# Kernel optimization log

Hardware: AMD Instinct MI355X
Metric: run time of the kernel (lower is better)

## Reference

```python
import jax, jax.numpy as jnp
import numpy as np

N, E = 30000, 480000
IN_DIM, HID, HEADS, OUT_DIM, EDIM = 128, 64, 4, 32, 1
NEG_SLOPE = 0.2
EPS_BN = 1e-5


def segment_softmax(logits, seg, num_segments):
    m = jax.ops.segment_max(logits, seg, num_segments=num_segments)
    ex = jnp.exp(logits - m[seg])
    s = jax.ops.segment_sum(ex, seg, num_segments=num_segments)
    return ex / (s[seg] + 1e-16)


def gat_layer(x, src, dst, ea, W, We, a_s, a_d, a_e, b):
    # PyG GATConv: shared lin for src/dst, edge_dim attention, softmax over dst
    n = x.shape[0]
    H, D = a_s.shape
    h = (x @ W).reshape(n, H, D)                      # [N,H,D]
    e = (ea @ We).reshape(-1, H, D)                   # [E,H,D]
    logits = (h * a_s).sum(-1)[src] + (h * a_d).sum(-1)[dst] + (e * a_e).sum(-1)
    alpha = segment_softmax(jax.nn.leaky_relu(logits, NEG_SLOPE), dst, n)  # [E,H]
    out = jax.ops.segment_sum(alpha[:, :, None] * h[src], dst, num_segments=n)
    return out.reshape(n, H * D) + b


def setup_inputs() -> dict:
    key = jax.random.key(0)
    ks = jax.random.split(key, 24)
    s = 0.1
    return {
        "x": jax.random.normal(ks[0], (N, IN_DIM), jnp.float32),
        "edge_attr": jax.random.uniform(ks[1], (E, EDIM), jnp.float32),
        "bn_gamma": jnp.ones((EDIM,), jnp.float32),
        "bn_beta": jnp.zeros((EDIM,), jnp.float32),
        "W1": s * jax.random.normal(ks[2], (IN_DIM, HEADS * HID), jnp.float32),
        "We1": s * jax.random.normal(ks[3], (EDIM, HEADS * HID), jnp.float32),
        "a_src1": s * jax.random.normal(ks[4], (HEADS, HID), jnp.float32),
        "a_dst1": s * jax.random.normal(ks[5], (HEADS, HID), jnp.float32),
        "a_edge1": s * jax.random.normal(ks[6], (HEADS, HID), jnp.float32),
        "b1": jnp.zeros((HEADS * HID,), jnp.float32),
        "W2": s * jax.random.normal(ks[7], (HEADS * HID, OUT_DIM), jnp.float32),
        "We2": s * jax.random.normal(ks[8], (EDIM, OUT_DIM), jnp.float32),
        "a_src2": s * jax.random.normal(ks[9], (1, OUT_DIM), jnp.float32),
        "a_dst2": s * jax.random.normal(ks[10], (1, OUT_DIM), jnp.float32),
        "a_edge2": s * jax.random.normal(ks[11], (1, OUT_DIM), jnp.float32),
        "b2": jnp.zeros((OUT_DIM,), jnp.float32),
        "dec_W1": s * jax.random.normal(ks[12], (OUT_DIM, HID), jnp.float32),
        "dec_b1": jnp.zeros((HID,), jnp.float32),
        "dec_W2": s * jax.random.normal(ks[13], (HID, IN_DIM), jnp.float32),
        "dec_b2": jnp.zeros((IN_DIM,), jnp.float32),
        "edge_index": jax.random.randint(ks[14], (2, E), 0, N, dtype=jnp.int32),
    }


def reference(x, edge_attr, bn_gamma, bn_beta, W1, We1, a_src1, a_dst1, a_edge1, b1,
              W2, We2, a_src2, a_dst2, a_edge2, b2, dec_W1, dec_b1, dec_W2, dec_b2,
              edge_index):
    n = x.shape[0]
    src, dst = edge_index[0], edge_index[1]
    # BatchNorm1d (batch stats, biased var) on log1p(edge_attr)
    ea = jnp.log1p(edge_attr)
    mu = ea.mean(0)
    var = ea.var(0)
    ea = (ea - mu) / jnp.sqrt(var + EPS_BN) * bn_gamma + bn_beta
    # add_self_loops with fill_value='mean' (mean of incoming edge attrs per node)
    ones = jnp.ones((src.shape[0],), ea.dtype)
    cnt = jax.ops.segment_sum(ones, dst, num_segments=n)
    loop_attr = jax.ops.segment_sum(ea, dst, num_segments=n) / jnp.maximum(cnt, 1.0)[:, None]
    ar = jnp.arange(n)
    src2 = jnp.concatenate([src, ar])
    dst2 = jnp.concatenate([dst, ar])
    ea2 = jnp.concatenate([ea, loop_attr], axis=0)
    # encoder: 2-layer GAT (eval mode: dropout is identity)
    h = jax.nn.elu(gat_layer(x, src2, dst2, ea2, W1, We1, a_src1, a_dst1, a_edge1, b1))
    z = gat_layer(h, src2, dst2, ea2, W2, We2, a_src2, a_dst2, a_edge2, b2)
    # feature decoder MLP
    x_hat = jax.nn.elu(z @ dec_W1 + dec_b1) @ dec_W2 + dec_b2
    return z, x_hat
```

## Files before the change

### kernel.cpp

```cpp
#include <hip/hip_runtime.h>
#include <math.h>

#define NN 30000
#define EE 480000
#define NEG_SLOPE 0.2f
#define LDK 136
#define LDK2 264
#define CAP 64
#define NPB 1875

static const size_t I_FILL  = 0;
static const size_t F_PART  = 30000;
static const size_t F_SCAL  = 34096;
static const size_t F_WTB   = 34112;
static const size_t F_WT2B  = 50496;
static const size_t F_HB    = 54592;
static const size_t F_S1    = 3894592;
static const size_t F_D1    = 4014592;
static const size_t F_H1B   = 4134592;
static const size_t F_H2    = 7974592;
static const size_t F_S2    = 8934592;
static const size_t F_D2    = 8964592;
static const size_t I_ER    = 8994592;

typedef __attribute__((ext_vector_type(4))) float f32x4;
typedef __attribute__((ext_vector_type(8))) short bf16x8;

__device__ __forceinline__ float wsum64(float v) {
    #pragma unroll
    for (int o = 32; o; o >>= 1) v += __shfl_xor(v, o);
    return v;
}
__device__ __forceinline__ unsigned int pack_bf2(float a, float b) {
    unsigned int ua = __float_as_uint(a);
    unsigned int ub = __float_as_uint(b);
    ua = (ua + 0x7FFFu + ((ua >> 16) & 1u)) >> 16;
    ub = (ub + 0x7FFFu + ((ub >> 16) & 1u)) & 0xFFFF0000u;
    return ua | ub;
}
__device__ __forceinline__ unsigned short bf16r(float f) {
    unsigned int u = __float_as_uint(f);
    u = (u + 0x7FFFu + ((u >> 16) & 1u)) >> 16;
    return (unsigned short)u;
}
__device__ __forceinline__ float bflo(unsigned int u) { return __uint_as_float(u << 16); }
__device__ __forceinline__ float bfhi(unsigned int u) { return __uint_as_float(u & 0xFFFF0000u); }

__global__ __launch_bounds__(256) void k_prepw(const float* __restrict__ W1,
        const float* __restrict__ W2, unsigned short* __restrict__ wtb,
        unsigned short* __restrict__ wt2b, int* __restrict__ fill) {
    int idx = blockIdx.x * 256 + threadIdx.x;
    if (idx < NN) fill[idx] = 0;
    if (idx < 128 * 256) {
        int k = idx >> 8, n = idx & 255;
        wtb[n * 128 + k] = bf16r(W1[idx]);
    } else if (idx < 128 * 256 + 256 * 32) {
        int i2 = idx - 128 * 256;
        int k = i2 >> 5, c = i2 & 31;
        wt2b[c * 256 + k] = bf16r(W2[i2]);
    }
}

__global__ __launch_bounds__(256) void k_scatter(const int* __restrict__ src,
        const int* __restrict__ dst, const float* __restrict__ eattr,
        int* __restrict__ fill, uint2* __restrict__ er,
        float* __restrict__ part, int E) {
    __shared__ float sa[256], sb[256];
    int tid = threadIdx.x;
    int e = blockIdx.x * 256 + tid;
    float s = 0.f, s2 = 0.f;
    if (e < E) {
        float lv = log1pf(eattr[e]);
        s = lv; s2 = lv * lv;
        int d = dst[e];
        int pos = atomicAdd(&fill[d], 1);
        if (pos > CAP - 2) pos = CAP - 2;
        er[d * CAP + pos] = make_uint2((unsigned int)src[e], __float_as_uint(lv));
    }
    sa[tid] = s; sb[tid] = s2;
    __syncthreads();
    for (int o = 128; o; o >>= 1) {
        if (tid < o) { sa[tid] += sa[tid + o]; sb[tid] += sb[tid + o]; }
        __syncthreads();
    }
    if (tid == 0) { part[blockIdx.x * 2] = sa[0]; part[blockIdx.x * 2 + 1] = sb[0]; }
}

__global__ __launch_bounds__(512) void k_bn_final(const float* __restrict__ part,
        const float* __restrict__ gamma, const float* __restrict__ beta,
        const float* __restrict__ We1, const float* __restrict__ ae1,
        const float* __restrict__ We2, const float* __restrict__ ae2,
        float* __restrict__ scal, int E) {
    __shared__ float sa[512], sb[512], sc[256];
    int tid = threadIdx.x;
    float s = 0.f, s2 = 0.f;
    for (int i = tid; i < NPB; i += 512) {
        s += part[2 * i]; s2 += part[2 * i + 1];
    }
    sa[tid] = s; sb[tid] = s2;
    if (tid < 256) sc[tid] = We1[tid] * ae1[tid];
    __syncthreads();
    for (int o = 256; o; o >>= 1) {
        if (tid < o) { sa[tid] += sa[tid + o]; sb[tid] += sb[tid + o]; }
        __syncthreads();
    }
    if (tid == 0) {
        float mu = sa[0] / (float)E;
        float var = sb[0] / (float)E - mu * mu;
        float kA = gamma[0] / sqrtf(var + 1e-5f);
        float kB = beta[0] - mu * kA;
        for (int h = 0; h < 4; h++) {
            float s1 = 0.f;
            for (int d = 0; d < 64; d++) s1 += sc[h * 64 + d];
            scal[4 + h] = kA * s1;
            scal[10 + h] = kB * s1;
        }
        float s22 = 0.f;
        for (int d = 0; d < 32; d++) s22 += We2[d] * ae2[d];
        scal[8] = kA * s22;
        scal[9] = kB * s22;
    }
}

__global__ __launch_bounds__(256) void k_gemm1(const float* __restrict__ x,
        const unsigned short* __restrict__ wtb, const float* __restrict__ as1,
        const float* __restrict__ ad1, unsigned short* __restrict__ hb,
        float* __restrict__ s1, float* __restrict__ d1, int M) {
    __shared__ unsigned short xs[32 * LDK];
    __shared__ unsigned short wt[256 * LDK];
    int tid = threadIdx.x;
    int bm = blockIdx.x * 32;
    #pragma unroll
    for (int i = 0; i < 16; i++) {
        int c = tid + i * 256;
        int row = c >> 4, koff = (c & 15) * 8;
        uint4 v = *(const uint4*)&wtb[row * 128 + koff];
        *(uint4*)&wt[row * LDK + koff] = v;
    }
    #pragma unroll
    for (int i = 0; i < 4; i++) {
        int idx = tid + i * 256;
        int row = idx >> 5, c4 = (idx & 31) * 4;
        int grow = bm + row;
        float4 v = make_float4(0.f, 0.f, 0.f, 0.f);
        if (grow < M) v = *(const float4*)&x[grow * 128 + c4];
        uint2 p = make_uint2(pack_bf2(v.x, v.y), pack_bf2(v.z, v.w));
        *(uint2*)&xs[row * LDK + c4] = p;
    }
    __syncthreads();

    int w = tid >> 6;
    int l = tid & 63;
    int l15 = l & 15, lg = l >> 4;

    f32x4 acc[2][4];
    #pragma unroll
    for (int m = 0; m < 2; m++)
        #pragma unroll
        for (int n = 0; n < 4; n++) acc[m][n] = (f32x4){0.f, 0.f, 0.f, 0.f};

    #pragma unroll
    for (int ks = 0; ks < 4; ks++) {
        int k0 = ks * 32 + lg * 8;
        bf16x8 a0 = *(const bf16x8*)&xs[(l15) * LDK + k0];
        bf16x8 a1 = *(const bf16x8*)&xs[(16 + l15) * LDK + k0];
        bf16x8 b[4];
        #pragma unroll
        for (int n = 0; n < 4; n++)
            b[n] = *(const bf16x8*)&wt[(w * 64 + n * 16 + l15) * LDK + k0];
        #pragma unroll
        for (int n = 0; n < 4; n++) {
            acc[0][n] = __builtin_amdgcn_mfma_f32_16x16x32_bf16(a0, b[n], acc[0][n], 0, 0, 0);
            acc[1][n] = __builtin_amdgcn_mfma_f32_16x16x32_bf16(a1, b[n], acc[1][n], 0, 0, 0);
        }
    }

    #pragma unroll
    for (int m = 0; m < 2; m++) {
        #pragma unroll
        for (int r = 0; r < 4; r++) {
            int grow = bm + m * 16 + lg * 4 + r;
            if (grow < M) {
                #pragma unroll
                for (int n = 0; n < 4; n++)
                    hb[grow * 256 + w * 64 + n * 16 + l15] = bf16r(acc[m][n][r]);
            }
        }
    }
    float as_c[4], ad_c[4];
    #pragma unroll
    for (int n = 0; n < 4; n++) {
        as_c[n] = as1[w * 64 + n * 16 + l15];
        ad_c[n] = ad1[w * 64 + n * 16 + l15];
    }
    float sp[2][4], dp[2][4];
    #pragma unroll
    for (int m = 0; m < 2; m++)
        #pragma unroll
        for (int r = 0; r < 4; r++) {
            float s = 0.f, d = 0.f;
            #pragma unroll
            for (int n = 0; n < 4; n++) {
                s += acc[m][n][r] * as_c[n];
                d += acc[m][n][r] * ad_c[n];
            }
            sp[m][r] = s; dp[m][r] = d;
        }
    #pragma unroll
    for (int o = 1; o < 16; o <<= 1) {
        #pragma unroll
        for (int m = 0; m < 2; m++)
            #pragma unroll
            for (int r = 0; r < 4; r++) {
                sp[m][r] += __shfl_xor(sp[m][r], o);
                dp[m][r] += __shfl_xor(dp[m][r], o);
            }
    }
    if (l15 == 0) {
        #pragma unroll
        for (int m = 0; m < 2; m++)
            #pragma unroll
            for (int r = 0; r < 4; r++) {
                int grow = bm + m * 16 + lg * 4 + r;
                if (grow < M) {
                    s1[grow * 4 + w] = sp[m][r];
                    d1[grow * 4 + w] = dp[m][r];
                }
            }
    }
}

__global__ __launch_bounds__(256) void k_agg1(const int* __restrict__ fill,
        const uint2* __restrict__ er, const float* __restrict__ s1,
        const float* __restrict__ d1, const float* __restrict__ scal,
        const unsigned short* __restrict__ hb, const float* __restrict__ b1,
        unsigned short* __restrict__ h1b, int N) {
    __shared__ float sma[4][256];
    __shared__ int   sms[4][64];
    int wid = threadIdx.x >> 6;
    int node = blockIdx.x * 4 + wid;
    if (node >= N) return;
    int lane = threadIdx.x & 63;
    int deg = fill[node]; if (deg > 63) deg = 63;
    float4 dv = *(const float4*)&d1[node * 4];
    float4 ce = *(const float4*)&scal[4];
    float4 cc = *(const float4*)&scal[10];

    uint2 e = make_uint2((unsigned int)node, 0u);
    if (lane < deg) e = er[node * CAP + lane];
    float ev = (lane < deg) ? __uint_as_float(e.y) : 0.f;
    float evm = wsum64(ev) / fmaxf((float)deg, 1.f);
    int degT = deg + 1;
    if (lane == deg) ev = evm;
    bool valid = lane < degT;

    float4 l = make_float4(-1e30f, -1e30f, -1e30f, -1e30f);
    if (valid) {
        float4 sv = *(const float4*)&s1[e.x * 4];
        l.x = sv.x + dv.x + ev * ce.x + cc.x;
        l.y = sv.y + dv.y + ev * ce.y + cc.y;
        l.z = sv.z + dv.z + ev * ce.z + cc.z;
        l.w = sv.w + dv.w + ev * ce.w + cc.w;
        l.x = l.x > 0.f ? l.x : NEG_SLOPE * l.x;
        l.y = l.y > 0.f ? l.y : NEG_SLOPE * l.y;
        l.z = l.z > 0.f ? l.z : NEG_SLOPE * l.z;
        l.w = l.w > 0.f ? l.w : NEG_SLOPE * l.w;
    }
    float4 mx = l;
    #pragma unroll
    for (int o = 32; o; o >>= 1) {
        mx.x = fmaxf(mx.x, __shfl_xor(mx.x, o));
        mx.y = fmaxf(mx.y, __shfl_xor(mx.y, o));
        mx.z = fmaxf(mx.z, __shfl_xor(mx.z, o));
        mx.w = fmaxf(mx.w, __shfl_xor(mx.w, o));
    }
    float4 ex = make_float4(0.f, 0.f, 0.f, 0.f);
    if (valid) {
        ex.x = __expf(l.x - mx.x); ex.y = __expf(l.y - mx.y);
        ex.z = __expf(l.z - mx.z); ex.w = __expf(l.w - mx.w);
    }
    float4 sm = ex;
    #pragma unroll
    for (int o = 32; o; o >>= 1) {
        sm.x += __shfl_xor(sm.x, o); sm.y += __shfl_xor(sm.y, o);
        sm.z += __shfl_xor(sm.z, o); sm.w += __shfl_xor(sm.w, o);
    }
    *(float4*)&sma[wid][lane * 4] = make_float4(ex.x, ex.y, ex.z, ex.w);
    sms[wid][lane] = (int)e.x;
    int p = lane >> 5;
    int dL = lane & 31;
    int h = dL >> 3;
    float acc[8];
    #pragma unroll
    for (int i = 0; i < 8; i++) acc[i] = 0.f;
    for (int c0 = 0; c0 < degT; c0 += 8) {
        int sv[4]; float av[4];
        #pragma unroll
        for (int t = 0; t < 4; t++) {
            int ee = c0 + 2 * t + p;
            sv[t] = sms[wid][ee];
            av[t] = sma[wid][ee * 4 + h];
        }
        uint4 hv[4];
        #pragma unroll
        for (int t = 0; t < 4; t++)
            hv[t] = *(const uint4*)&hb[(unsigned)sv[t] * 256 + dL * 8];
        #pragma unroll
        for (int t = 0; t < 4; t++) {
            float a = av[t];
            acc[0] += a * bflo(hv[t].x); acc[1] += a * bfhi(hv[t].x);
            acc[2] += a * bflo(hv[t].y); acc[3] += a * bfhi(hv[t].y);
            acc[4] += a * bflo(hv[t].z); acc[5] += a * bfhi(hv[t].z);
            acc[6] += a * bflo(hv[t].w); acc[7] += a * bfhi(hv[t].w);
        }
    }
    #pragma unroll
    for (int i = 0; i < 8; i++) acc[i] += __shfl_xor(acc[i], 32);
    float smh = h == 0 ? sm.x : h == 1 ? sm.y : h == 2 ? sm.z : sm.w;
    float invh = 1.f / (smh + 1e-16f);
    float4 bb0 = *(const float4*)&b1[dL * 8];
    float4 bb1 = *(const float4*)&b1[dL * 8 + 4];
    float r[8];
    r[0] = acc[0] * invh + bb0.x; r[1] = acc[1] * invh + bb0.y;
    r[2] = acc[2] * invh + bb0.z; r[3] = acc[3] * invh + bb0.w;
    r[4] = acc[4] * invh + bb1.x; r[5] = acc[5] * invh + bb1.y;
    r[6] = acc[6] * invh + bb1.z; r[7] = acc[7] * invh + bb1.w;
    #pragma unroll
    for (int i = 0; i < 8; i++)
        r[i] = r[i] > 0.f ? r[i] : (__expf(r[i]) - 1.f);
    if (p == 0) {
        uint4 pk;
        pk.x = pack_bf2(r[0], r[1]); pk.y = pack_bf2(r[2], r[3]);
        pk.z = pack_bf2(r[4], r[5]); pk.w = pack_bf2(r[6], r[7]);
        *(uint4*)&h1b[node * 256 + dL * 8] = pk;
    }
}

__global__ __launch_bounds__(256) void k_gemm2(const unsigned short* __restrict__ h1b,
        const unsigned short* __restrict__ wt2b, const float* __restrict__ as2,
        const float* __restrict__ ad2, float* __restrict__ h2,
        float* __restrict__ s2, float* __restrict__ d2, int M) {
    __shared__ unsigned short h1s[64 * LDK2];
    __shared__ unsigned short w2s[32 * LDK2];
    int tid = threadIdx.x;
    int bm = blockIdx.x * 64;
    #pragma unroll
    for (int i = 0; i < 8; i++) {
        int c = tid + i * 256;
        int row = c >> 5, off = (c & 31) * 8;
        int grow = bm + row;
        uint4 v = make_uint4(0u, 0u, 0u, 0u);
        if (grow < M) v = *(const uint4*)&h1b[grow * 256 + off];
        *(uint4*)&h1s[row * LDK2 + off] = v;
    }
    #pragma unroll
    for (int i = 0; i < 4; i++) {
        int c = tid + i * 256;
        int row = c >> 5, off = (c & 31) * 8;
        uint4 v = *(const uint4*)&wt2b[row * 256 + off];
        *(uint4*)&w2s[row * LDK2 + off] = v;
    }
    __syncthreads();

    int w = tid >> 6;
    int l = tid & 63;
    int l15 = l & 15, lg = l >> 4;

    f32x4 acc0 = (f32x4){0.f, 0.f, 0.f, 0.f};
    f32x4 acc1 = (f32x4){0.f, 0.f, 0.f, 0.f};
    #pragma unroll
    for (int ks = 0; ks < 8; ks++) {
        int k0 = ks * 32 + lg * 8;
        bf16x8 a = *(const bf16x8*)&h1s[(w * 16 + l15) * LDK2 + k0];
        bf16x8 b0 = *(const bf16x8*)&w2s[(l15) * LDK2 + k0];
        bf16x8 b1 = *(const bf16x8*)&w2s[(16 + l15) * LDK2 + k0];
        acc0 = __builtin_amdgcn_mfma_f32_16x16x32_bf16(a, b0, acc0, 0, 0, 0);
        acc1 = __builtin_amdgcn_mfma_f32_16x16x32_bf16(a, b1, acc1, 0, 0, 0);
    }

    #pragma unroll
    for (int r = 0; r < 4; r++) {
        int grow = bm + w * 16 + lg * 4 + r;
        if (grow < M) {
            h2[grow * 32 + l15] = acc0[r];
            h2[grow * 32 + 16 + l15] = acc1[r];
        }
    }
    float sc0 = as2[l15], sc1 = as2[16 + l15];
    float dc0 = ad2[l15], dc1 = ad2[16 + l15];
    #pragma unroll
    for (int r = 0; r < 4; r++) {
        float sp = acc0[r] * sc0 + acc1[r] * sc1;
        float dp = acc0[r] * dc0 + acc1[r] * dc1;
        #pragma unroll
        for (int o = 1; o < 16; o <<= 1) {
            sp += __shfl_xor(sp, o);
            dp += __shfl_xor(dp, o);
        }
        if (l15 == 0) {
            int grow = bm + w * 16 + lg * 4 + r;
            if (grow < M) { s2[grow] = sp; d2[grow] = dp; }
        }
    }
}

__global__ __launch_bounds__(256) void k_agg2(const int* __restrict__ fill,
        const uint2* __restrict__ er, const float* __restrict__ s2,
        const float* __restrict__ d2, const float* __restrict__ scal,
        const float* __restrict__ h2, const float* __restrict__ b2,
        float* __restrict__ zout, int N) {
    __shared__ float sa2[4][64];
    __shared__ int   ss2[4][64];
    int wid = threadIdx.x >> 6;
    int node = blockIdx.x * 4 + wid;
    if (node >= N) return;
    int lane = threadIdx.x & 63;
    int deg = fill[node]; if (deg > 63) deg = 63;
    float dn = d2[node];
    float ce = scal[8], cc = scal[9];

    uint2 e = make_uint2((unsigned int)node, 0u);
    if (lane < deg) e = er[node * CAP + lane];
    float ev = (lane < deg) ? __uint_as_float(e.y) : 0.f;
    float evm = wsum64(ev) / fmaxf((float)deg, 1.f);
    int degT = deg + 1;
    if (lane == deg) ev = evm;
    bool valid = lane < degT;

    float l = -1e30f;
    if (valid) {
        l = s2[e.x] + dn + ev * ce + cc;
        l = l > 0.f ? l : NEG_SLOPE * l;
    }
    float mx = l;
    #pragma unroll
    for (int o = 32; o; o >>= 1) mx = fmaxf(mx, __shfl_xor(mx, o));
    float ex = valid ? __expf(l - mx) : 0.f;
    float sm = wsum64(ex);
    float inv = 1.f / (sm + 1e-16f);
    sa2[wid][lane] = ex;
    ss2[wid][lane] = (int)e.x;
    int p8 = lane >> 3, dL2 = lane & 7;
    float4 acc = make_float4(0.f, 0.f, 0.f, 0.f);
    for (int c0 = 0; c0 < degT; c0 += 32) {
        int sv[4]; float av[4];
        #pragma unroll
        for (int t = 0; t < 4; t++) {
            int ee = c0 + 8 * t + p8;
            sv[t] = ss2[wid][ee];
            av[t] = sa2[wid][ee];
        }
        float4 hv[4];
        #pragma unroll
        for (int t = 0; t < 4; t++)
            hv[t] = *(const float4*)&h2[(unsigned)sv[t] * 32 + dL2 * 4];
        #pragma unroll
        for (int t = 0; t < 4; t++) {
            acc.x += av[t] * hv[t].x; acc.y += av[t] * hv[t].y;
            acc.z += av[t] * hv[t].z; acc.w += av[t] * hv[t].w;
        }
    }
    #pragma unroll
    for (int o = 8; o <= 32; o <<= 1) {
        acc.x += __shfl_xor(acc.x, o); acc.y += __shfl_xor(acc.y, o);
        acc.z += __shfl_xor(acc.z, o); acc.w += __shfl_xor(acc.w, o);
    }
    if (lane < 8) {
        float4 bb = *(const float4*)&b2[dL2 * 4];
        float4 oo;
        oo.x = acc.x * inv + bb.x; oo.y = acc.y * inv + bb.y;
        oo.z = acc.z * inv + bb.z; oo.w = acc.w * inv + bb.w;
        *(float4*)&zout[node * 32 + dL2 * 4] = oo;
    }
}

__global__ __launch_bounds__(256) void k_decoder(const float* __restrict__ z,
        const float* __restrict__ W1, const float* __restrict__ b1,
        const float* __restrict__ W2, const float* __restrict__ b2,
        float* __restrict__ xhat, int M) {
    __shared__ float zs[16][32];
    __shared__ float w1s[32 * 64];
    __shared__ float hid[16][68];
    __shared__ float w2s[64 * 128];
    int tid = threadIdx.x;
    int bn = blockIdx.x * 16;
    #pragma unroll
    for (int i = 0; i < 2; i++) {
        int idx = tid + i * 256;
        int r = idx >> 5, c = idx & 31;
        int row = bn + r;
        zs[r][c] = (row < M) ? z[row * 32 + c] : 0.f;
    }
    #pragma unroll
    for (int i = 0; i < 2; i++) {
        int idx = tid + i * 256;
        int r = idx >> 4, c = (idx & 15) * 4;
        *(float4*)&w1s[r * 64 + c] = *(const float4*)&W1[r * 64 + c];
    }
    #pragma unroll
    for (int i = 0; i < 8; i++) {
        int idx = tid + i * 256;
        int r = idx >> 5, c = (idx & 31) * 4;
        *(float4*)&w2s[r * 128 + c] = *(const float4*)&W2[r * 128 + c];
    }
    __syncthreads();
    {
        int nl = tid >> 4, c0 = (tid & 15) * 4;
        float4 acc = make_float4(0.f, 0.f, 0.f, 0.f);
        #pragma unroll 8
        for (int k = 0; k < 32; k++) {
            float zv = zs[nl][k];
            float4 w = *(float4*)&w1s[k * 64 + c0];
            acc.x += zv * w.x; acc.y += zv * w.y;
            acc.z += zv * w.z; acc.w += zv * w.w;
        }
        float4 bb = *(const float4*)&b1[c0];
        float r0 = acc.x + bb.x, r1 = acc.y + bb.y, r2 = acc.z + bb.z, r3 = acc.w + bb.w;
        r0 = r0 > 0.f ? r0 : (__expf(r0) - 1.f);
        r1 = r1 > 0.f ? r1 : (__expf(r1) - 1.f);
        r2 = r2 > 0.f ? r2 : (__expf(r2) - 1.f);
        r3 = r3 > 0.f ? r3 : (__expf(r3) - 1.f);
        hid[nl][c0] = r0; hid[nl][c0 + 1] = r1; hid[nl][c0 + 2] = r2; hid[nl][c0 + 3] = r3;
    }
    __syncthreads();
    {
        int nl = tid >> 4, c0 = (tid & 15) * 4;
        float acc[8];
        #pragma unroll
        for (int q = 0; q < 8; q++) acc[q] = 0.f;
        #pragma unroll 8
        for (int k = 0; k < 64; k++) {
            float hv = hid[nl][k];
            float4 w0 = *(float4*)&w2s[k * 128 + c0];
            float4 w1 = *(float4*)&w2s[k * 128 + c0 + 64];
            acc[0] += hv * w0.x; acc[1] += hv * w0.y; acc[2] += hv * w0.z; acc[3] += hv * w0.w;
            acc[4] += hv * w1.x; acc[5] += hv * w1.y; acc[6] += hv * w1.z; acc[7] += hv * w1.w;
        }
        int row = bn + nl;
        if (row < M) {
            float4 bb0 = *(const float4*)&b2[c0];
            float4 bb1 = *(const float4*)&b2[c0 + 64];
            float4 o0 = make_float4(acc[0] + bb0.x, acc[1] + bb0.y, acc[2] + bb0.z, acc[3] + bb0.w);
            float4 o1 = make_float4(acc[4] + bb1.x, acc[5] + bb1.y, acc[6] + bb1.z, acc[7] + bb1.w);
            *(float4*)&xhat[row * 128 + c0] = o0;
            *(float4*)&xhat[row * 128 + c0 + 64] = o1;
        }
    }
}

extern "C" void kernel_launch(void* const* d_in, const int* in_sizes, int n_in,
                              void* d_out, int out_size, void* d_ws, size_t ws_size,
                              hipStream_t stream) {
    const float* x        = (const float*)d_in[0];
    const float* eattr    = (const float*)d_in[1];
    const float* bn_gamma = (const float*)d_in[2];
    const float* bn_beta  = (const float*)d_in[3];
    const float* W1       = (const float*)d_in[4];
    const float* We1      = (const float*)d_in[5];
    const float* as1      = (const float*)d_in[6];
    const float* ad1      = (const float*)d_in[7];
    const float* ae1      = (const float*)d_in[8];
    const float* b1       = (const float*)d_in[9];
    const float* W2       = (const float*)d_in[10];
    const float* We2      = (const float*)d_in[11];
    const float* as2      = (const float*)d_in[12];
    const float* ad2      = (const float*)d_in[13];
    const float* ae2      = (const float*)d_in[14];
    const float* b2       = (const float*)d_in[15];
    const float* dW1      = (const float*)d_in[16];
    const float* db1      = (const float*)d_in[17];
    const float* dW2      = (const float*)d_in[18];
    const float* db2      = (const float*)d_in[19];
    const int*   eidx     = (const int*)d_in[20];
    const int* src = eidx;
    const int* dst = eidx + EE;

    float* ws = (float*)d_ws;
    int*   fill = (int*)(ws + I_FILL);
    float* part = ws + F_PART;
    float* scal = ws + F_SCAL;
    unsigned short* wtb  = (unsigned short*)(ws + F_WTB);
    unsigned short* wt2b = (unsigned short*)(ws + F_WT2B);
    unsigned short* hb   = (unsigned short*)(ws + F_HB);
    float* s1   = ws + F_S1;
    float* d1   = ws + F_D1;
    unsigned short* h1b = (unsigned short*)(ws + F_H1B);
    float* h2   = ws + F_H2;
    float* s2   = ws + F_S2;
    float* d2   = ws + F_D2;
    uint2* er   = (uint2*)(ws + I_ER);

    float* zout = (float*)d_out;
    float* xhat = (float*)d_out + NN * 32;

    k_prepw<<<160, 256, 0, stream>>>(W1, W2, wtb, wt2b, fill);
    k_scatter<<<NPB, 256, 0, stream>>>(src, dst, eattr, fill, er, part, EE);
    k_bn_final<<<1, 512, 0, stream>>>(part, bn_gamma, bn_beta, We1, ae1, We2, ae2, scal, EE);
    k_gemm1<<<(NN + 31) / 32, 256, 0, stream>>>(x, wtb, as1, ad1, hb, s1, d1, NN);
    k_agg1<<<(NN + 3) / 4, 256, 0, stream>>>(fill, er, s1, d1, scal, hb, b1, h1b, NN);
    k_gemm2<<<(NN + 63) / 64, 256, 0, stream>>>(h1b, wt2b, as2, ad2, h2, s2, d2, NN);
    k_agg2<<<(NN + 3) / 4, 256, 0, stream>>>(fill, er, s2, d2, scal, h2, b2, zout, NN);
    k_decoder<<<(NN + 15) / 16, 256, 0, stream>>>(zout, dW1, db1, dW2, db2, xhat, NN);
}
```

Measured before the change: 136.5 us.

## Merge edge scatter and first-layer GEMM into one launch via block ranges

Combines the edge scatter/BN-partial kernel and the layer-1 GEMM into a single grid, where the first NPB blocks do the scatter and the remaining blocks do the GEMM. The two independent stages can then overlap on the GPU and one launch disappears. The GEMM also stops staging the whole 256x128 weight tile in LDS and reads B fragments directly from global/L2, which cuts LDS use to raise occupancy. The cost is uncoalesced, repeated global reads of the weights in the MFMA loop.

New measurement: 135.0 us. No clear change (-1.1%).

```diff
diff --git a/kernel.cpp b/kernel.cpp
--- a/kernel.cpp
+++ b/kernel.cpp
@@ -8,6 +8,7 @@
 #define LDK2 264
 #define CAP 64
 #define NPB 1875
+#define NGB 938
 
 static const size_t I_FILL  = 0;
 static const size_t F_PART  = 30000;
@@ -61,29 +62,132 @@
     }
 }
 
-__global__ __launch_bounds__(256) void k_scatter(const int* __restrict__ src,
+__global__ __launch_bounds__(256) void k_scat_gemm(const int* __restrict__ src,
         const int* __restrict__ dst, const float* __restrict__ eattr,
-        int* __restrict__ fill, uint2* __restrict__ er,
-        float* __restrict__ part, int E) {
-    __shared__ float sa[256], sb[256];
+        int* __restrict__ fill, uint2* __restrict__ er, float* __restrict__ part,
+        const float* __restrict__ x, const unsigned short* __restrict__ wtb,
+        const float* __restrict__ as1, const float* __restrict__ ad1,
+        unsigned short* __restrict__ hb, float* __restrict__ s1,
+        float* __restrict__ d1, int E, int M) {
+    __shared__ char shbuf[32 * LDK * 2];
     int tid = threadIdx.x;
-    int e = blockIdx.x * 256 + tid;
-    float s = 0.f, s2 = 0.f;
-    if (e < E) {
-        float lv = log1pf(eattr[e]);
-        s = lv; s2 = lv * lv;
-        int d = dst[e];
-        int pos = atomicAdd(&fill[d], 1);
-        if (pos > CAP - 2) pos = CAP - 2;
-        er[d * CAP + pos] = make_uint2((unsigned int)src[e], __float_as_uint(lv));
-    }
-    sa[tid] = s; sb[tid] = s2;
+
+    if (blockIdx.x < NPB) {
+        float* sa = (float*)shbuf;
+        float* sb = sa + 256;
+        int e = blockIdx.x * 256 + tid;
+        float s = 0.f, s2 = 0.f;
+        if (e < E) {
+            float lv = log1pf(eattr[e]);
+            s = lv; s2 = lv * lv;
+            int d = dst[e];
+            int pos = atomicAdd(&fill[d], 1);
+            if (pos > CAP - 2) pos = CAP - 2;
+            er[d * CAP + pos] = make_uint2((unsigned int)src[e], __float_as_uint(lv));
+        }
+        sa[tid] = s; sb[tid] = s2;
+        __syncthreads();
+        for (int o = 128; o; o >>= 1) {
+            if (tid < o) { sa[tid] += sa[tid + o]; sb[tid] += sb[tid + o]; }
+            __syncthreads();
+        }
+        if (tid == 0) { part[blockIdx.x * 2] = sa[0]; part[blockIdx.x * 2 + 1] = sb[0]; }
+        return;
+    }
+
+    unsigned short* xs = (unsigned short*)shbuf;
+    int bm = (blockIdx.x - NPB) * 32;
+    #pragma unroll
+    for (int i = 0; i < 4; i++) {
+        int idx = tid + i * 256;
+        int row = idx >> 5, c4 = (idx & 31) * 4;
+        int grow = bm + row;
+        float4 v = make_float4(0.f, 0.f, 0.f, 0.f);
+        if (grow < M) v = *(const float4*)&x[grow * 128 + c4];
+        uint2 p = make_uint2(pack_bf2(v.x, v.y), pack_bf2(v.z, v.w));
+        *(uint2*)&xs[row * LDK + c4] = p;
+    }
     __syncthreads();
-    for (int o = 128; o; o >>= 1) {
-        if (tid < o) { sa[tid] += sa[tid + o]; sb[tid] += sb[tid + o]; }
-        __syncthreads();
-    }
-    if (tid == 0) { part[blockIdx.x * 2] = sa[0]; part[blockIdx.x * 2 + 1] = sb[0]; }
+
+    int w = tid >> 6;
+    int l = tid & 63;
+    int l15 = l & 15, lg = l >> 4;
+
+    f32x4 acc[2][4];
+    #pragma unroll
+    for (int m = 0; m < 2; m++)
+        #pragma unroll
+        for (int n = 0; n < 4; n++) acc[m][n] = (f32x4){0.f, 0.f, 0.f, 0.f};
+
+    #pragma unroll
+    for (int ks = 0; ks < 4; ks++) {
+        int k0 = ks * 32 + lg * 8;
+        bf16x8 a0 = *(const bf16x8*)&xs[(l15) * LDK + k0];
+        bf16x8 a1 = *(const bf16x8*)&xs[(16 + l15) * LDK + k0];
+        bf16x8 b[4];
+        #pragma unroll
+        for (int n = 0; n < 4; n++)
+            b[n] = *(const bf16x8*)&wtb[(w * 64 + n * 16 + l15) * 128 + k0];
+        #pragma unroll
+        for (int n = 0; n < 4; n++) {
+            acc[0][n] = __builtin_amdgcn_mfma_f32_16x16x32_bf16(a0, b[n], acc[0][n], 0, 0, 0);
+            acc[1][n] = __builtin_amdgcn_mfma_f32_16x16x32_bf16(a1, b[n], acc[1][n], 0, 0, 0);
+        }
+    }
+
+    #pragma unroll
+    for (int m = 0; m < 2; m++) {
+        #pragma unroll
+        for (int r = 0; r < 4; r++) {
+            int grow = bm + m * 16 + lg * 4 + r;
+            if (grow < M) {
+                #pragma unroll
+                for (int n = 0; n < 4; n++)
+                    hb[grow * 256 + w * 64 + n * 16 + l15] = bf16r(acc[m][n][r]);
+            }
+        }
+    }
+    float as_c[4], ad_c[4];
+    #pragma unroll
+    for (int n = 0; n < 4; n++) {
+        as_c[n] = as1[w * 64 + n * 16 + l15];
+        ad_c[n] = ad1[w * 64 + n * 16 + l15];
+    }
+    float sp[2][4], dp[2][4];
+    #pragma unroll
+    for (int m = 0; m < 2; m++)
+        #pragma unroll
+        for (int r = 0; r < 4; r++) {
+            float s = 0.f, d = 0.f;
+            #pragma unroll
+            for (int n = 0; n < 4; n++) {
+                s += acc[m][n][r] * as_c[n];
+                d += acc[m][n][r] * ad_c[n];
+            }
+            sp[m][r] = s; dp[m][r] = d;
+        }
+    #pragma unroll
+    for (int o = 1; o < 16; o <<= 1) {
+        #pragma unroll
+        for (int m = 0; m < 2; m++)
+            #pragma unroll
+            for (int r = 0; r < 4; r++) {
+                sp[m][r] += __shfl_xor(sp[m][r], o);
+                dp[m][r] += __shfl_xor(dp[m][r], o);
+            }
+    }
+    if (l15 == 0) {
+        #pragma unroll
+        for (int m = 0; m < 2; m++)
+            #pragma unroll
+            for (int r = 0; r < 4; r++) {
+                int grow = bm + m * 16 + lg * 4 + r;
+                if (grow < M) {
+                    s1[grow * 4 + w] = sp[m][r];
+                    d1[grow * 4 + w] = dp[m][r];
+                }
+            }
+    }
 }
 
 __global__ __launch_bounds__(512) void k_bn_final(const float* __restrict__ part,
@@ -119,114 +223,6 @@
         for (int d = 0; d < 32; d++) s22 += We2[d] * ae2[d];
         scal[8] = kA * s22;
         scal[9] = kB * s22;
-    }
-}
-
-__global__ __launch_bounds__(256) void k_gemm1(const float* __restrict__ x,
-        const unsigned short* __restrict__ wtb, const float* __restrict__ as1,
-        const float* __restrict__ ad1, unsigned short* __restrict__ hb,
-        float* __restrict__ s1, float* __restrict__ d1, int M) {
-    __shared__ unsigned short xs[32 * LDK];
-    __shared__ unsigned short wt[256 * LDK];
-    int tid = threadIdx.x;
-    int bm = blockIdx.x * 32;
-    #pragma unroll
-    for (int i = 0; i < 16; i++) {
-        int c = tid + i * 256;
-        int row = c >> 4, koff = (c & 15) * 8;
-        uint4 v = *(const uint4*)&wtb[row * 128 + koff];
-        *(uint4*)&wt[row * LDK + koff] = v;
-    }
-    #pragma unroll
-    for (int i = 0; i < 4; i++) {
-        int idx = tid + i * 256;
-        int row = idx >> 5, c4 = (idx & 31) * 4;
-        int grow = bm + row;
-        float4 v = make_float4(0.f, 0.f, 0.f, 0.f);
-        if (grow < M) v = *(const float4*)&x[grow * 128 + c4];
-        uint2 p = make_uint2(pack_bf2(v.x, v.y), pack_bf2(v.z, v.w));
-        *(uint2*)&xs[row * LDK + c4] = p;
-    }
-    __syncthreads();
-
-    int w = tid >> 6;
-    int l = tid & 63;
-    int l15 = l & 15, lg = l >> 4;
-
-    f32x4 acc[2][4];
-    #pragma unroll
-    for (int m = 0; m < 2; m++)
-        #pragma unroll
-        for (int n = 0; n < 4; n++) acc[m][n] = (f32x4){0.f, 0.f, 0.f, 0.f};
-
-    #pragma unroll
-    for (int ks = 0; ks < 4; ks++) {
-        int k0 = ks * 32 + lg * 8;
-        bf16x8 a0 = *(const bf16x8*)&xs[(l15) * LDK + k0];
-        bf16x8 a1 = *(const bf16x8*)&xs[(16 + l15) * LDK + k0];
-        bf16x8 b[4];
-        #pragma unroll
-        for (int n = 0; n < 4; n++)
-            b[n] = *(const bf16x8*)&wt[(w * 64 + n * 16 + l15) * LDK + k0];
-        #pragma unroll
-        for (int n = 0; n < 4; n++) {
-            acc[0][n] = __builtin_amdgcn_mfma_f32_16x16x32_bf16(a0, b[n], acc[0][n], 0, 0, 0);
-            acc[1][n] = __builtin_amdgcn_mfma_f32_16x16x32_bf16(a1, b[n], acc[1][n], 0, 0, 0);
-        }
-    }
-
-    #pragma unroll
-    for (int m = 0; m < 2; m++) {
-        #pragma unroll
-        for (int r = 0; r < 4; r++) {
-            int grow = bm + m * 16 + lg * 4 + r;
-            if (grow < M) {
-                #pragma unroll
-                for (int n = 0; n < 4; n++)
-                    hb[grow * 256 + w * 64 + n * 16 + l15] = bf16r(acc[m][n][r]);
-            }
-        }
-    }
-    float as_c[4], ad_c[4];
-    #pragma unroll
-    for (int n = 0; n < 4; n++) {
-        as_c[n] = as1[w * 64 + n * 16 + l15];
-        ad_c[n] = ad1[w * 64 + n * 16 + l15];
-    }
-    float sp[2][4], dp[2][4];
-    #pragma unroll
-    for (int m = 0; m < 2; m++)
-        #pragma unroll
-        for (int r = 0; r < 4; r++) {
-            float s = 0.f, d = 0.f;
-            #pragma unroll
-            for (int n = 0; n < 4; n++) {
-                s += acc[m][n][r] * as_c[n];
-                d += acc[m][n][r] * ad_c[n];
-            }
-            sp[m][r] = s; dp[m][r] = d;
-        }
-    #pragma unroll
-    for (int o = 1; o < 16; o <<= 1) {
-        #pragma unroll
-        for (int m = 0; m < 2; m++)
-            #pragma unroll
-            for (int r = 0; r < 4; r++) {
-                sp[m][r] += __shfl_xor(sp[m][r], o);
-                dp[m][r] += __shfl_xor(dp[m][r], o);
-            }
-    }
-    if (l15 == 0) {
-        #pragma unroll
-        for (int m = 0; m < 2; m++)
-            #pragma unroll
-            for (int r = 0; r < 4; r++) {
-                int grow = bm + m * 16 + lg * 4 + r;
-                if (grow < M) {
-                    s1[grow * 4 + w] = sp[m][r];
-                    d1[grow * 4 + w] = dp[m][r];
-                }
-            }
     }
 }
 
@@ -594,9 +590,9 @@
     float* xhat = (float*)d_out + NN * 32;
 
     k_prepw<<<160, 256, 0, stream>>>(W1, W2, wtb, wt2b, fill);
-    k_scatter<<<NPB, 256, 0, stream>>>(src, dst, eattr, fill, er, part, EE);
+    k_scat_gemm<<<NPB + NGB, 256, 0, stream>>>(src, dst, eattr, fill, er, part,
+                                               x, wtb, as1, ad1, hb, s1, d1, EE, NN);
     k_bn_final<<<1, 512, 0, stream>>>(part, bn_gamma, bn_beta, We1, ae1, We2, ae2, scal, EE);
-    k_gemm1<<<(NN + 31) / 32, 256, 0, stream>>>(x, wtb, as1, ad1, hb, s1, d1, NN);
     k_agg1<<<(NN + 3) / 4, 256, 0, stream>>>(fill, er, s1, d1, scal, hb, b1, h1b, NN);
     k_gemm2<<<(NN + 63) / 64, 256, 0, stream>>>(h1b, wt2b, as2, ad2, h2, s2, d2, NN);
     k_agg2<<<(NN + 3) / 4, 256, 0, stream>>>(fill, er, s2, d2, scal, h2, b2, zout, NN);
```
